# Performance work log

Measured on AMD Instinct MI355X. Metric: run time of the kernel, lower is better.

Reference implementation:

```python
import jax, jax.numpy as jnp
import numpy as np

C = 4096      # channels_in == channels_out == Cn (deg rows)
K = 3         # dynamic kernel size
RED = 8       # CA reduction
CH, CW = 64, 64  # reshape_codebooks(4096) -> (sqrt(4096), sqrt(4096)); must equal feature H, W


def leaky(x):
    return jnp.where(x >= 0, x, 0.1 * x)  # LeakyReLU(0.1)


def setup_inputs() -> dict:
    key = jax.random.key(0)
    ks = jax.random.split(key, 8)
    s = 0.02
    return {
        "c": jax.random.normal(ks[0], (1, C, CH, CW), jnp.float32),      # feature map B,C,H,W (B=1 required)
        "deg": jax.random.normal(ks[1], (C, C), jnp.float32),            # degradation reps Cn x C
        "W1": jax.random.normal(ks[2], (C, C), jnp.float32) * s,         # kernel MLP: Linear(C,C,bias=False) weight (out,in)
        "W2": jax.random.normal(ks[3], (K * K, C), jnp.float32) * s,     # kernel MLP: Linear(C,K*K,bias=False)
        "Wc": jax.random.normal(ks[4], (C, C), jnp.float32) * s,         # 1x1 conv weight (out,in)
        "bc": jnp.zeros((C,), jnp.float32),                              # 1x1 conv bias
        "Wd1": jax.random.normal(ks[5], (C // RED, C), jnp.float32) * s, # CA conv1 1x1 (out,in)
        "Wd2": jax.random.normal(ks[6], (C, C // RED), jnp.float32) * s, # CA conv2 1x1 (out,in)
    }


def reference(c, deg, W1, W2, Wc, bc, Wd1, Wd2):
    b, cc, h, w = c.shape
    # --- dynamic per-channel kernel generation: Linear -> LeakyReLU -> Linear ---
    kern = leaky(deg @ W1.T) @ W2.T                      # (b*c, K*K)
    kern = kern.reshape(b * cc, 1, K, K)                 # depthwise weights (O, 1, K, K)
    # --- depthwise grouped conv with groups = b*c ---
    pad = (K - 1) // 2
    x = c.reshape(1, b * cc, h, w)
    out = jax.lax.conv_general_dilated(
        x, kern, window_strides=(1, 1), padding=((pad, pad), (pad, pad)),
        feature_group_count=b * cc, dimension_numbers=('NCHW', 'OIHW', 'NCHW'))
    out = leaky(out).reshape(b, cc, h, w)
    # --- 1x1 conv (channels_in -> channels_out) ---
    out = jnp.einsum('oc,bchw->bohw', Wc, out) + bc[None, :, None, None]
    # --- channel attention branch on deg ---
    d = deg.reshape(1, C, CH, CW)
    hid = leaky(jnp.einsum('oc,bchw->bohw', Wd1, d))     # (1, C//RED, CH, CW)
    att = jax.nn.sigmoid(jnp.einsum('oc,bchw->bohw', Wd2, hid))  # (1, C, CH, CW)
    return out + d * att
```

## Files before the change

kernel.cpp:

```cpp
#include <hip/hip_runtime.h>
#include <stdint.h>

typedef unsigned short u16;
typedef __attribute__((ext_vector_type(8))) short bf16x8;
typedef __attribute__((ext_vector_type(4))) float f32x4;

static __device__ __forceinline__ u16 f2bf(float f) {
  uint32_t u = __float_as_uint(f);
  return (u16)((u + 0x7fffu + ((u >> 16) & 1u)) >> 16);
}
static __device__ __forceinline__ float bf2f(u16 h) {
  return __uint_as_float(((uint32_t)h) << 16);
}

static __device__ __forceinline__ void gload_lds16(const void* g, void* l) {
  __builtin_amdgcn_global_load_lds((const __attribute__((address_space(1))) void*)g,
                                   (__attribute__((address_space(3))) void*)l, 16, 0, 0);
}

__global__ __launch_bounds__(256) void cast_bf16_kernel(const float* __restrict__ in,
                                                        u16* __restrict__ out, int n4) {
  int idx = blockIdx.x * 256 + threadIdx.x;
  if (idx >= n4) return;
  float4 v = ((const float4*)in)[idx];
  u16 o0 = f2bf(v.x), o1 = f2bf(v.y), o2 = f2bf(v.z), o3 = f2bf(v.w);
  uint2 packed;
  packed.x = (uint32_t)o0 | ((uint32_t)o1 << 16);
  packed.y = (uint32_t)o2 | ((uint32_t)o3 << 16);
  ((uint2*)out)[idx] = packed;
}

__global__ __launch_bounds__(256) void deg_prep_kernel(const float* __restrict__ in,
                                                       u16* __restrict__ degb,
                                                       u16* __restrict__ degt) {
  __shared__ float t[64][72];
  const int r0 = blockIdx.y * 64, c0 = blockIdx.x * 64;
  const int tid = threadIdx.x;
  const int rr = tid >> 4;
  const int c4 = (tid & 15) * 4;
#pragma unroll
  for (int s = 0; s < 4; ++s) {
    const int row = r0 + rr + s * 16;
    float4 v = *(const float4*)&in[(size_t)row * 4096 + c0 + c4];
    *(float4*)&t[rr + s * 16][c4] = v;
    uint2 p;
    p.x = (uint32_t)f2bf(v.x) | ((uint32_t)f2bf(v.y) << 16);
    p.y = (uint32_t)f2bf(v.z) | ((uint32_t)f2bf(v.w) << 16);
    *(uint2*)&degb[(size_t)row * 4096 + c0 + c4] = p;
  }
  __syncthreads();
  const int oc = tid >> 2;
  const int or16 = (tid & 3) * 16;
  bf16x8 o0, o1;
#pragma unroll
  for (int u = 0; u < 8; ++u) o0[u] = (short)f2bf(t[or16 + u][oc]);
#pragma unroll
  for (int u = 0; u < 8; ++u) o1[u] = (short)f2bf(t[or16 + 8 + u][oc]);
  *(bf16x8*)&degt[(size_t)(c0 + oc) * 4096 + r0 + or16] = o0;
  *(bf16x8*)&degt[(size_t)(c0 + oc) * 4096 + r0 + or16 + 8] = o1;
}

__global__ __launch_bounds__(256) void transpose_bf16_kernel(const u16* __restrict__ in,
                                                             u16* __restrict__ out) {
  __shared__ u16 t[64][72];
  const int r0 = blockIdx.y * 64, c0 = blockIdx.x * 64;
  const int tid = threadIdx.x;
  const int rr = tid >> 3;
  const int c8 = (tid & 7) * 8;
#pragma unroll
  for (int s = 0; s < 2; ++s) {
    bf16x8 v = *(const bf16x8*)&in[(size_t)(r0 + rr + s * 32) * 4096 + c0 + c8];
    *(bf16x8*)&t[rr + s * 32][c8] = v;
  }
  __syncthreads();
  const int oc = tid >> 2;
  const int or16 = (tid & 3) * 16;
  bf16x8 o0, o1;
#pragma unroll
  for (int u = 0; u < 8; ++u) o0[u] = (short)t[or16 + u][oc];
#pragma unroll
  for (int u = 0; u < 8; ++u) o1[u] = (short)t[or16 + 8 + u][oc];
  *(bf16x8*)&out[(size_t)(c0 + oc) * 4096 + r0 + or16] = o0;
  *(bf16x8*)&out[(size_t)(c0 + oc) * 4096 + r0 + or16 + 8] = o1;
}

__global__ __launch_bounds__(256) void combine_leaky_kernel(const float* __restrict__ P,
                                                            u16* __restrict__ out, int n4) {
  int idx = blockIdx.x * 256 + threadIdx.x;
  if (idx >= n4) return;
  float4 a = ((const float4*)P)[idx];
  float4 b = ((const float4*)(P + (size_t)4096 * 512))[idx];
  float s0 = a.x + b.x, s1 = a.y + b.y, s2 = a.z + b.z, s3 = a.w + b.w;
  s0 = s0 >= 0.f ? s0 : 0.1f * s0;
  s1 = s1 >= 0.f ? s1 : 0.1f * s1;
  s2 = s2 >= 0.f ? s2 : 0.1f * s2;
  s3 = s3 >= 0.f ? s3 : 0.1f * s3;
  uint2 p;
  p.x = (uint32_t)f2bf(s0) | ((uint32_t)f2bf(s1) << 16);
  p.y = (uint32_t)f2bf(s2) | ((uint32_t)f2bf(s3) << 16);
  ((uint2*)out)[idx] = p;
}

__global__ __launch_bounds__(256) void kern_reduce_kernel(const u16* __restrict__ H,
                                                          const float* __restrict__ W2,
                                                          float* __restrict__ kern) {
  const int i = blockIdx.x;
  const int tid = threadIdx.x;
  float acc[9];
#pragma unroll
  for (int t = 0; t < 9; ++t) acc[t] = 0.f;
#pragma unroll
  for (int it = 0; it < 2; ++it) {
    const int j = (it * 256 + tid) * 8;
    bf16x8 hv = *(const bf16x8*)&H[(size_t)i * 4096 + j];
    float hf[8];
#pragma unroll
    for (int u = 0; u < 8; ++u) hf[u] = bf2f((u16)hv[u]);
#pragma unroll
    for (int t = 0; t < 9; ++t) {
      float s = 0.f;
#pragma unroll
      for (int u = 0; u < 8; ++u) s += hf[u] * W2[t * 4096 + j + u];
      acc[t] += s;
    }
  }
  __shared__ float red[4 * 9];
  const int lane = tid & 63, wid = tid >> 6;
#pragma unroll
  for (int t = 0; t < 9; ++t) {
    float v = acc[t];
#pragma unroll
    for (int off = 32; off > 0; off >>= 1) v += __shfl_down(v, off);
    if (lane == 0) red[wid * 9 + t] = v;
  }
  __syncthreads();
  if (tid < 9) kern[(size_t)i * 9 + tid] = red[tid] + red[9 + tid] + red[18 + tid] + red[27 + tid];
}

__global__ __launch_bounds__(256) void dwconv_kernel(const float* __restrict__ x,
                                                     const float* __restrict__ kern,
                                                     u16* __restrict__ V) {
  const int ch = blockIdx.x;
  __shared__ float img[4096];
  const float* src = x + (size_t)ch * 4096;
#pragma unroll
  for (int s = 0; s < 4; ++s)
    ((float4*)img)[s * 256 + threadIdx.x] = ((const float4*)src)[s * 256 + threadIdx.x];
  float kv[9];
#pragma unroll
  for (int t = 0; t < 9; ++t) kv[t] = kern[(size_t)ch * 9 + t];
  __syncthreads();
#pragma unroll
  for (int s = 0; s < 16; ++s) {
    const int p = s * 256 + threadIdx.x;
    const int h = p >> 6, w = p & 63;
    float sum = 0.f;
#pragma unroll
    for (int dh = -1; dh <= 1; ++dh) {
      const int hh = h + dh;
      if ((unsigned)hh < 64u) {
#pragma unroll
        for (int dw = -1; dw <= 1; ++dw) {
          const int wwi = w + dw;
          if ((unsigned)wwi < 64u) sum += img[hh * 64 + wwi] * kv[(dh + 1) * 3 + (dw + 1)];
        }
      }
    }
    sum = sum >= 0.f ? sum : 0.1f * sum;
    V[(size_t)ch * 4096 + p] = f2bf(sum);
  }
}

template <int EPI>
__global__ __launch_bounds__(256, 4) void gemm_nt(const u16* __restrict__ A,
                                                  const u16* __restrict__ B,
                                                  void* __restrict__ Cout,
                                                  int M, int N, int K,
                                                  const float* __restrict__ bias,
                                                  const float* __restrict__ degf,
                                                  const u16* __restrict__ att) {
  __shared__ u16 Asm[128 * 64];
  __shared__ u16 Bsm[128 * 64];
  const int tid = threadIdx.x;
  const int lane = tid & 63;
  const int wid = tid >> 6;
  const int wr = wid >> 1, wc = wid & 1;
  const int nwg = gridDim.x * gridDim.y;
  int lin = blockIdx.y * gridDim.x + blockIdx.x;
  lin = (lin & 7) * (nwg >> 3) + (lin >> 3);
  const int bn = (lin % gridDim.x) * 128;
  const int bm = (lin / gridDim.x) * 128;
  const int kper = K / gridDim.z;
  const int k0 = blockIdx.z * kper, k1 = k0 + kper;

  const int srow = tid >> 3;
  const int sseg = tid & 7;
  const int ssw  = (sseg ^ (srow & 7)) * 8;
  const int l15 = lane & 15;
  const int seg0 = lane >> 4;
  const int lx7 = l15 & 7;

  f32x4 acc[4][4];
#pragma unroll
  for (int m = 0; m < 4; ++m)
#pragma unroll
    for (int n = 0; n < 4; ++n) acc[m][n] = (f32x4){0.f, 0.f, 0.f, 0.f};

  const size_t aBase = (size_t)bm * K;
  const size_t bBase = (size_t)bn * K;

  for (int kt = k0; kt < k1; kt += 64) {
    __syncthreads();
#pragma unroll
    for (int bi = 0; bi < 4; ++bi) {
      const u16* ga = A + aBase + (size_t)(bi * 32 + srow) * K + kt + ssw;
      gload_lds16(ga, &Asm[(bi * 32 + srow) * 64 + sseg * 8]);
      const u16* gb = B + bBase + (size_t)(bi * 32 + srow) * K + kt + ssw;
      gload_lds16(gb, &Bsm[(bi * 32 + srow) * 64 + sseg * 8]);
    }
    __syncthreads();
#pragma unroll
    for (int ks = 0; ks < 2; ++ks) {
      bf16x8 av[4], bv[4];
#pragma unroll
      for (int m = 0; m < 4; ++m)
        av[m] = *(const bf16x8*)&Asm[(wr * 64 + m * 16 + l15) * 64 +
                                     (((ks * 4 + seg0) ^ lx7) * 8)];
#pragma unroll
      for (int n = 0; n < 4; ++n)
        bv[n] = *(const bf16x8*)&Bsm[(wc * 64 + n * 16 + l15) * 64 +
                                     (((ks * 4 + seg0) ^ lx7) * 8)];
#pragma unroll
      for (int m = 0; m < 4; ++m)
#pragma unroll
        for (int n = 0; n < 4; ++n)
          acc[m][n] = __builtin_amdgcn_mfma_f32_16x16x32_bf16(av[m], bv[n], acc[m][n], 0, 0, 0);
    }
  }

#pragma unroll
  for (int m = 0; m < 4; ++m) {
    const int row0 = bm + wr * 64 + m * 16 + (lane >> 4) * 4;
#pragma unroll
    for (int n = 0; n < 4; ++n) {
      const int col = bn + wc * 64 + n * 16 + l15;
#pragma unroll
      for (int j = 0; j < 4; ++j) {
        const int row = row0 + j;
        float v = acc[m][n][j];
        const size_t idx = (size_t)row * N + col;
        if (EPI == 0) {
          v = v >= 0.f ? v : 0.1f * v;
          ((u16*)Cout)[idx] = f2bf(v);
        } else if (EPI == 1) {
          v = 1.f / (1.f + __expf(-v));
          ((u16*)Cout)[idx] = f2bf(v);
        } else if (EPI == 2) {
          v += bias[row] + degf[idx] * bf2f(att[idx]);
          ((float*)Cout)[idx] = v;
        } else {
          ((float*)Cout)[(size_t)blockIdx.z * ((size_t)M * N) + idx] = v;
        }
      }
    }
  }
}

extern "C" void kernel_launch(void* const* d_in, const int* in_sizes, int n_in,
                              void* d_out, int out_size, void* d_ws, size_t ws_size,
                              hipStream_t stream) {
  const float* xc  = (const float*)d_in[0];
  const float* deg = (const float*)d_in[1];
  const float* W1  = (const float*)d_in[2];
  const float* W2  = (const float*)d_in[3];
  const float* Wc  = (const float*)d_in[4];
  const float* bc  = (const float*)d_in[5];
  const float* Wd1 = (const float*)d_in[6];
  const float* Wd2 = (const float*)d_in[7];
  float* out = (float*)d_out;

  char* ws = (char*)d_ws;
  const size_t MB = 1ull << 20;
  u16* RA    = (u16*)(ws + 0 * MB);
  u16* RB    = (u16*)(ws + 32 * MB);
  u16* RC    = (u16*)(ws + 64 * MB);
  u16* ATT   = (u16*)(ws + 96 * MB);
  u16* WD1B  = (u16*)(ws + 128 * MB);
  u16* WD2B  = (u16*)(ws + 132 * MB);
  u16* HIDT  = (u16*)(ws + 136 * MB);
  float* KERN = (float*)(ws + 140 * MB);

  cast_bf16_kernel<<<2048, 256, 0, stream>>>(Wd1, WD1B, 512 * 4096 / 4);
  cast_bf16_kernel<<<2048, 256, 0, stream>>>(Wd2, WD2B, 4096 * 512 / 4);
  deg_prep_kernel<<<dim3(64, 64), 256, 0, stream>>>(deg, RB, RA);
  gemm_nt<3><<<dim3(4, 32, 2), 256, 0, stream>>>(RA, WD1B, (float*)RC, 4096, 512, 4096,
                                                 nullptr, nullptr, nullptr);
  combine_leaky_kernel<<<2048, 256, 0, stream>>>((const float*)RC, HIDT, 4096 * 512 / 4);
  gemm_nt<1><<<dim3(32, 32), 256, 0, stream>>>(WD2B, HIDT, ATT, 4096, 4096, 512,
                                               nullptr, nullptr, nullptr);

  cast_bf16_kernel<<<16384, 256, 0, stream>>>(W1, RA, 4096 * 4096 / 4);
  gemm_nt<0><<<dim3(32, 32), 256, 0, stream>>>(RB, RA, RC, 4096, 4096, 4096,
                                               nullptr, nullptr, nullptr);
  kern_reduce_kernel<<<4096, 256, 0, stream>>>(RC, W2, KERN);

  dwconv_kernel<<<4096, 256, 0, stream>>>(xc, KERN, RA);
  transpose_bf16_kernel<<<dim3(64, 64), 256, 0, stream>>>(RA, RB);

  cast_bf16_kernel<<<16384, 256, 0, stream>>>(Wc, RC, 4096 * 4096 / 4);
  gemm_nt<2><<<dim3(32, 32), 256, 0, stream>>>(RC, RB, out, 4096, 4096, 4096,
                                               bc, deg, ATT);
}
```

Baseline: 492.7 us.

## Fuse W2 kernel reduction into GEMM epilogue and read deg as bf16

The W1 GEMM epilogue now applies LeakyReLU and immediately contracts each row tile with W2. It writes 9-wide partial sums per column slice, and a small kernel sums the 64 slices. This replaces the full 4096x4096 bf16 hidden matrix write, its re-read and the old per-row reduction kernel. The final GEMM epilogue reads the bf16 copy of deg instead of the fp32 input, halving that traffic at some precision cost. The Wd1 GEMM also goes to 4-way split-K with a 4-slice combine. The fused epilogue adds per-element FMAs against W2 loads from global memory, plus cross-lane shuffles.

```diff
diff --git a/kernel.cpp b/kernel.cpp
--- a/kernel.cpp
+++ b/kernel.cpp
@@ -88,9 +88,15 @@
                                                             u16* __restrict__ out, int n4) {
   int idx = blockIdx.x * 256 + threadIdx.x;
   if (idx >= n4) return;
+  const size_t SL = (size_t)4096 * 512;
   float4 a = ((const float4*)P)[idx];
-  float4 b = ((const float4*)(P + (size_t)4096 * 512))[idx];
-  float s0 = a.x + b.x, s1 = a.y + b.y, s2 = a.z + b.z, s3 = a.w + b.w;
+  float4 b = ((const float4*)(P + SL))[idx];
+  float4 c = ((const float4*)(P + 2 * SL))[idx];
+  float4 d = ((const float4*)(P + 3 * SL))[idx];
+  float s0 = (a.x + b.x) + (c.x + d.x);
+  float s1 = (a.y + b.y) + (c.y + d.y);
+  float s2 = (a.z + b.z) + (c.z + d.z);
+  float s3 = (a.w + b.w) + (c.w + d.w);
   s0 = s0 >= 0.f ? s0 : 0.1f * s0;
   s1 = s1 >= 0.f ? s1 : 0.1f * s1;
   s2 = s2 >= 0.f ? s2 : 0.1f * s2;
@@ -101,40 +107,14 @@
   ((uint2*)out)[idx] = p;
 }
 
-__global__ __launch_bounds__(256) void kern_reduce_kernel(const u16* __restrict__ H,
-                                                          const float* __restrict__ W2,
-                                                          float* __restrict__ kern) {
-  const int i = blockIdx.x;
-  const int tid = threadIdx.x;
-  float acc[9];
-#pragma unroll
-  for (int t = 0; t < 9; ++t) acc[t] = 0.f;
-#pragma unroll
-  for (int it = 0; it < 2; ++it) {
-    const int j = (it * 256 + tid) * 8;
-    bf16x8 hv = *(const bf16x8*)&H[(size_t)i * 4096 + j];
-    float hf[8];
-#pragma unroll
-    for (int u = 0; u < 8; ++u) hf[u] = bf2f((u16)hv[u]);
-#pragma unroll
-    for (int t = 0; t < 9; ++t) {
-      float s = 0.f;
-#pragma unroll
-      for (int u = 0; u < 8; ++u) s += hf[u] * W2[t * 4096 + j + u];
-      acc[t] += s;
-    }
-  }
-  __shared__ float red[4 * 9];
-  const int lane = tid & 63, wid = tid >> 6;
-#pragma unroll
-  for (int t = 0; t < 9; ++t) {
-    float v = acc[t];
-#pragma unroll
-    for (int off = 32; off > 0; off >>= 1) v += __shfl_down(v, off);
-    if (lane == 0) red[wid * 9 + t] = v;
-  }
-  __syncthreads();
-  if (tid < 9) kern[(size_t)i * 9 + tid] = red[tid] + red[9 + tid] + red[18 + tid] + red[27 + tid];
+__global__ __launch_bounds__(256) void kpart_reduce_kernel(const float* __restrict__ kp,
+                                                           float* __restrict__ kern) {
+  int idx = blockIdx.x * 256 + threadIdx.x;
+  if (idx >= 4096 * 9) return;
+  float s = 0.f;
+#pragma unroll
+  for (int sl = 0; sl < 64; ++sl) s += kp[(size_t)sl * 36864 + idx];
+  kern[idx] = s;
 }
 
 __global__ __launch_bounds__(256) void dwconv_kernel(const float* __restrict__ x,
@@ -177,8 +157,8 @@
                                                   void* __restrict__ Cout,
                                                   int M, int N, int K,
                                                   const float* __restrict__ bias,
-                                                  const float* __restrict__ degf,
-                                                  const u16* __restrict__ att) {
+                                                  const u16* __restrict__ att,
+                                                  const u16* __restrict__ degb) {
   __shared__ u16 Asm[128 * 64];
   __shared__ u16 Bsm[128 * 64];
   const int tid = threadIdx.x;
@@ -238,28 +218,57 @@
     }
   }
 
-#pragma unroll
-  for (int m = 0; m < 4; ++m) {
-    const int row0 = bm + wr * 64 + m * 16 + (lane >> 4) * 4;
-#pragma unroll
-    for (int n = 0; n < 4; ++n) {
-      const int col = bn + wc * 64 + n * 16 + l15;
-#pragma unroll
-      for (int j = 0; j < 4; ++j) {
-        const int row = row0 + j;
-        float v = acc[m][n][j];
-        const size_t idx = (size_t)row * N + col;
-        if (EPI == 0) {
+  if (EPI == 4) {
+    const int g = lane >> 4;
+    float* kp = (float*)Cout + (size_t)((bn >> 7) * 2 + wc) * 36864;
+#pragma unroll
+    for (int m = 0; m < 4; ++m) {
+#pragma unroll
+      for (int jr = 0; jr < 4; ++jr) {
+        const int i = bm + wr * 64 + m * 16 + g * 4 + jr;
+        float s[9];
+#pragma unroll
+        for (int t = 0; t < 9; ++t) s[t] = 0.f;
+#pragma unroll
+        for (int n = 0; n < 4; ++n) {
+          float v = acc[m][n][jr];
           v = v >= 0.f ? v : 0.1f * v;
-          ((u16*)Cout)[idx] = f2bf(v);
-        } else if (EPI == 1) {
-          v = 1.f / (1.f + __expf(-v));
-          ((u16*)Cout)[idx] = f2bf(v);
-        } else if (EPI == 2) {
-          v += bias[row] + degf[idx] * bf2f(att[idx]);
-          ((float*)Cout)[idx] = v;
-        } else {
-          ((float*)Cout)[(size_t)blockIdx.z * ((size_t)M * N) + idx] = v;
+          const int col = bn + wc * 64 + n * 16 + l15;
+#pragma unroll
+          for (int t = 0; t < 9; ++t) s[t] += v * bias[t * 4096 + col];
+        }
+#pragma unroll
+        for (int off = 1; off < 16; off <<= 1) {
+#pragma unroll
+          for (int t = 0; t < 9; ++t) s[t] += __shfl_xor(s[t], off);
+        }
+        if (l15 == 0) {
+#pragma unroll
+          for (int t = 0; t < 9; ++t) kp[(size_t)i * 9 + t] = s[t];
+        }
+      }
+    }
+  } else {
+#pragma unroll
+    for (int m = 0; m < 4; ++m) {
+      const int row0 = bm + wr * 64 + m * 16 + (lane >> 4) * 4;
+#pragma unroll
+      for (int n = 0; n < 4; ++n) {
+        const int col = bn + wc * 64 + n * 16 + l15;
+#pragma unroll
+        for (int j = 0; j < 4; ++j) {
+          const int row = row0 + j;
+          float v = acc[m][n][j];
+          const size_t idx = (size_t)row * N + col;
+          if (EPI == 1) {
+            v = 1.f / (1.f + __expf(-v));
+            ((u16*)Cout)[idx] = f2bf(v);
+          } else if (EPI == 3) {
+            ((float*)Cout)[(size_t)blockIdx.z * ((size_t)M * N) + idx] = v;
+          } else {
+            v += bias[row] + bf2f(degb[idx]) * bf2f(att[idx]);
+            ((float*)Cout)[idx] = v;
+          }
         }
       }
     }
@@ -284,7 +293,7 @@
   u16* RA    = (u16*)(ws + 0 * MB);
   u16* RB    = (u16*)(ws + 32 * MB);
   u16* RC    = (u16*)(ws + 64 * MB);
-  u16* ATT   = (u16*)(ws + 96 * MB);
+  u16* RATT  = (u16*)(ws + 96 * MB);
   u16* WD1B  = (u16*)(ws + 128 * MB);
   u16* WD2B  = (u16*)(ws + 132 * MB);
   u16* HIDT  = (u16*)(ws + 136 * MB);
@@ -293,21 +302,21 @@
   cast_bf16_kernel<<<2048, 256, 0, stream>>>(Wd1, WD1B, 512 * 4096 / 4);
   cast_bf16_kernel<<<2048, 256, 0, stream>>>(Wd2, WD2B, 4096 * 512 / 4);
   deg_prep_kernel<<<dim3(64, 64), 256, 0, stream>>>(deg, RB, RA);
-  gemm_nt<3><<<dim3(4, 32, 2), 256, 0, stream>>>(RA, WD1B, (float*)RC, 4096, 512, 4096,
+  gemm_nt<3><<<dim3(4, 32, 4), 256, 0, stream>>>(RA, WD1B, (float*)RC, 4096, 512, 4096,
                                                  nullptr, nullptr, nullptr);
   combine_leaky_kernel<<<2048, 256, 0, stream>>>((const float*)RC, HIDT, 4096 * 512 / 4);
-  gemm_nt<1><<<dim3(32, 32), 256, 0, stream>>>(WD2B, HIDT, ATT, 4096, 4096, 512,
+  gemm_nt<1><<<dim3(32, 32), 256, 0, stream>>>(WD2B, HIDT, RATT, 4096, 4096, 512,
                                                nullptr, nullptr, nullptr);
 
   cast_bf16_kernel<<<16384, 256, 0, stream>>>(W1, RA, 4096 * 4096 / 4);
-  gemm_nt<0><<<dim3(32, 32), 256, 0, stream>>>(RB, RA, RC, 4096, 4096, 4096,
-                                               nullptr, nullptr, nullptr);
-  kern_reduce_kernel<<<4096, 256, 0, stream>>>(RC, W2, KERN);
+  gemm_nt<4><<<dim3(32, 32), 256, 0, stream>>>(RB, RA, (float*)RC, 4096, 4096, 4096,
+                                               W2, nullptr, nullptr);
+  kpart_reduce_kernel<<<144, 256, 0, stream>>>((const float*)RC, KERN);
 
   dwconv_kernel<<<4096, 256, 0, stream>>>(xc, KERN, RA);
-  transpose_bf16_kernel<<<dim3(64, 64), 256, 0, stream>>>(RA, RB);
-
-  cast_bf16_kernel<<<16384, 256, 0, stream>>>(Wc, RC, 4096 * 4096 / 4);
-  gemm_nt<2><<<dim3(32, 32), 256, 0, stream>>>(RC, RB, out, 4096, 4096, 4096,
-                                               bc, deg, ATT);
-}
+  transpose_bf16_kernel<<<dim3(64, 64), 256, 0, stream>>>(RA, RC);
+
+  cast_bf16_kernel<<<16384, 256, 0, stream>>>(Wc, RA, 4096 * 4096 / 4);
+  gemm_nt<5><<<dim3(32, 32), 256, 0, stream>>>(RA, RC, out, 4096, 4096, 4096,
+                                               bc, RATT, RB);
+}
```

Result: slower. 523.0 us (+6.2%).

## Add 256x256 eight-wave pipelined GEMM for deg@W1 and raise split-K for CA

Applied to the files above, without the earlier changes.

Replaces the generic gemm_nt<0> for the 4096^3 deg@W1 product with a new 256x256-tile, 512-thread kernel. It uses direct global-to-LDS loads with XOR-swizzled rows, double-buffered 128KB LDS, explicit waitcnt and barrier phasing, setprio around MFMA bursts, and a fused LeakyReLU bf16 epilogue. It also raises the split-K of the Wd1 GEMM from 2 to 4, with the combine kernel now summing four partials, and vectorises kern_reduce loads. The aim is better MFMA utilisation and latency hiding on the largest GEMM. The cost is one workgroup per CU and hand-tuned sync that depends on exact sizes.

```diff
diff --git a/kernel.cpp b/kernel.cpp
--- a/kernel.cpp
+++ b/kernel.cpp
@@ -16,6 +16,12 @@
 static __device__ __forceinline__ void gload_lds16(const void* g, void* l) {
   __builtin_amdgcn_global_load_lds((const __attribute__((address_space(1))) void*)g,
                                    (__attribute__((address_space(3))) void*)l, 16, 0, 0);
+}
+
+static __device__ __forceinline__ bf16x8 dsr128(uint32_t byteaddr) {
+  bf16x8 r;
+  asm volatile("ds_read_b128 %0, %1" : "=v"(r) : "v"(byteaddr));
+  return r;
 }
 
 __global__ __launch_bounds__(256) void cast_bf16_kernel(const float* __restrict__ in,
@@ -88,9 +94,15 @@
                                                             u16* __restrict__ out, int n4) {
   int idx = blockIdx.x * 256 + threadIdx.x;
   if (idx >= n4) return;
+  const size_t SL = (size_t)4096 * 512;
   float4 a = ((const float4*)P)[idx];
-  float4 b = ((const float4*)(P + (size_t)4096 * 512))[idx];
-  float s0 = a.x + b.x, s1 = a.y + b.y, s2 = a.z + b.z, s3 = a.w + b.w;
+  float4 b = ((const float4*)(P + SL))[idx];
+  float4 c = ((const float4*)(P + 2 * SL))[idx];
+  float4 d = ((const float4*)(P + 3 * SL))[idx];
+  float s0 = (a.x + b.x) + (c.x + d.x);
+  float s1 = (a.y + b.y) + (c.y + d.y);
+  float s2 = (a.z + b.z) + (c.z + d.z);
+  float s3 = (a.w + b.w) + (c.w + d.w);
   s0 = s0 >= 0.f ? s0 : 0.1f * s0;
   s1 = s1 >= 0.f ? s1 : 0.1f * s1;
   s2 = s2 >= 0.f ? s2 : 0.1f * s2;
@@ -110,18 +122,15 @@
 #pragma unroll
   for (int t = 0; t < 9; ++t) acc[t] = 0.f;
 #pragma unroll
-  for (int it = 0; it < 2; ++it) {
-    const int j = (it * 256 + tid) * 8;
-    bf16x8 hv = *(const bf16x8*)&H[(size_t)i * 4096 + j];
-    float hf[8];
-#pragma unroll
-    for (int u = 0; u < 8; ++u) hf[u] = bf2f((u16)hv[u]);
+  for (int it = 0; it < 4; ++it) {
+    const int j = it * 1024 + tid * 4;
+    uint2 hv = *(const uint2*)&H[(size_t)i * 4096 + j];
+    float h0 = bf2f((u16)(hv.x & 0xffff)), h1 = bf2f((u16)(hv.x >> 16));
+    float h2 = bf2f((u16)(hv.y & 0xffff)), h3 = bf2f((u16)(hv.y >> 16));
 #pragma unroll
     for (int t = 0; t < 9; ++t) {
-      float s = 0.f;
-#pragma unroll
-      for (int u = 0; u < 8; ++u) s += hf[u] * W2[t * 4096 + j + u];
-      acc[t] += s;
+      float4 w = *(const float4*)&W2[t * 4096 + j];
+      acc[t] += h0 * w.x + h1 * w.y + h2 * w.z + h3 * w.w;
     }
   }
   __shared__ float red[4 * 9];
@@ -266,6 +275,124 @@
   }
 }
 
+template __global__ void gemm_nt<0>(const u16*, const u16*, void*, int, int, int,
+                                    const float*, const float*, const u16*);
+
+#define PH4(P, BUFB, READB, S1, S2, TAILV)                                         \
+  {                                                                                \
+    bf16x8 af[4][2];                                                               \
+    _Pragma("unroll") for (int f = 0; f < 4; ++f) {                                \
+      af[f][0] = dsr128((BUFB) + arow + (uint32_t)(((P) * 4 + f) * 2048) + sg0);   \
+      af[f][1] = dsr128((BUFB) + arow + (uint32_t)(((P) * 4 + f) * 2048) + sg1);   \
+    }                                                                              \
+    if (READB) {                                                                   \
+      _Pragma("unroll") for (int nf = 0; nf < 4; ++nf) {                           \
+        bfr[nf][0] = dsr128((BUFB) + brow + (uint32_t)(nf * 2048) + sg0);          \
+        bfr[nf][1] = dsr128((BUFB) + brow + (uint32_t)(nf * 2048) + sg1);          \
+      }                                                                            \
+    }                                                                              \
+    S1; S2;                                                                        \
+    __builtin_amdgcn_s_barrier();                                                  \
+    asm volatile("s_waitcnt lgkmcnt(0)" ::: "memory");                             \
+    __builtin_amdgcn_sched_barrier(0);                                             \
+    __builtin_amdgcn_s_setprio(1);                                                 \
+    _Pragma("unroll") for (int f = 0; f < 4; ++f)                                  \
+      _Pragma("unroll") for (int nf = 0; nf < 4; ++nf)                             \
+        _Pragma("unroll") for (int ks = 0; ks < 2; ++ks)                           \
+          acc[(P) * 4 + f][nf] = __builtin_amdgcn_mfma_f32_16x16x32_bf16(          \
+              af[f][ks], bfr[nf][ks], acc[(P) * 4 + f][nf], 0, 0, 0);              \
+    __builtin_amdgcn_s_setprio(0);                                                 \
+    __builtin_amdgcn_sched_barrier(0);                                             \
+    TAILV;                                                                         \
+    __builtin_amdgcn_s_barrier();                                                  \
+  }
+#define VM4 asm volatile("s_waitcnt vmcnt(4)" ::: "memory")
+#define VM0 asm volatile("s_waitcnt vmcnt(0)" ::: "memory")
+
+__global__ __launch_bounds__(512, 1) void gemm8p4(const u16* __restrict__ A,
+                                                  const u16* __restrict__ B,
+                                                  u16* __restrict__ Cout,
+                                                  int N, int K, int gx) {
+  extern __shared__ u16 lds[];
+  const int tid = threadIdx.x;
+  const int lane = tid & 63;
+  const int w = tid >> 6;
+  const int wr = w >> 2, wcn = w & 3;
+
+  const int nwg = gridDim.x;
+  const int cpx = nwg >> 3;
+  const int swz = (blockIdx.x & 7) * cpx + (blockIdx.x >> 3);
+  const int bn = (swz % gx) * 256;
+  const int bm = (swz / gx) * 256;
+
+  const int srow = tid >> 3;
+  const int sseg = tid & 7;
+  const int ssrc = (sseg ^ (srow & 7)) * 8;
+
+  const int l15 = lane & 15, g = lane >> 4;
+  const uint32_t sg0 = (uint32_t)(((0 + g) ^ (l15 & 7)) * 16);
+  const uint32_t sg1 = (uint32_t)(((4 + g) ^ (l15 & 7)) * 16);
+  const uint32_t arow = (uint32_t)((wr * 128 + l15) * 128);
+  const uint32_t brow = (uint32_t)((wcn * 64 + l15) * 128) + 32768u;
+
+  const u16* Ab = A + (size_t)(bm + srow) * K + ssrc;
+  const u16* Bb = B + (size_t)(bn + srow) * K + ssrc;
+
+  auto stage = [&](const u16* Mb, uint32_t bufbyte, int t, int half) {
+#pragma unroll
+    for (int r = 0; r < 2; ++r) {
+      const int rowl = half * 128 + r * 64 + srow;
+      gload_lds16(Mb + (size_t)(half * 128 + r * 64) * K + (size_t)t * 64,
+                  (char*)lds + bufbyte + (uint32_t)(rowl * 128 + sseg * 16));
+    }
+  };
+
+  f32x4 acc[8][4];
+#pragma unroll
+  for (int m = 0; m < 8; ++m)
+#pragma unroll
+    for (int n = 0; n < 4; ++n) acc[m][n] = (f32x4){0.f, 0.f, 0.f, 0.f};
+  bf16x8 bfr[4][2];
+
+  const int NIT = K >> 7;
+
+  stage(Bb, 32768u, 0, 0); stage(Bb, 32768u, 0, 1);
+  stage(Ab, 0u, 0, 0);     stage(Ab, 0u, 0, 1);
+  stage(Bb, 98304u, 1, 0); stage(Bb, 98304u, 1, 1);
+  VM4;
+  __builtin_amdgcn_s_barrier();
+
+  for (int i = 0; i < NIT - 1; ++i) {
+    const int to = 2 * i + 1, te = 2 * i + 2, tn = 2 * i + 3;
+    PH4(0, 0u, 1, stage(Ab, 65536u, to, 0), stage(Ab, 65536u, to, 1), );
+    PH4(1, 0u, 0, stage(Bb, 32768u, te, 0), stage(Bb, 32768u, te, 1), VM4);
+    PH4(0, 65536u, 1, stage(Ab, 0u, te, 0), stage(Ab, 0u, te, 1), );
+    PH4(1, 65536u, 0, stage(Bb, 98304u, tn, 0), stage(Bb, 98304u, tn, 1), VM4);
+  }
+  {
+    const int to = 2 * (NIT - 1) + 1;
+    PH4(0, 0u, 1, stage(Ab, 65536u, to, 0), stage(Ab, 65536u, to, 1), );
+    PH4(1, 0u, 0, , , VM0);
+    PH4(0, 65536u, 1, , , );
+    PH4(1, 65536u, 0, , , );
+  }
+
+#pragma unroll
+  for (int mf = 0; mf < 8; ++mf) {
+    const int row0 = bm + wr * 128 + mf * 16 + (lane >> 4) * 4;
+#pragma unroll
+    for (int nf = 0; nf < 4; ++nf) {
+      const int col = bn + wcn * 64 + nf * 16 + l15;
+#pragma unroll
+      for (int j = 0; j < 4; ++j) {
+        float v = acc[mf][nf][j];
+        v = v >= 0.f ? v : 0.1f * v;
+        Cout[(size_t)(row0 + j) * N + col] = f2bf(v);
+      }
+    }
+  }
+}
+
 extern "C" void kernel_launch(void* const* d_in, const int* in_sizes, int n_in,
                               void* d_out, int out_size, void* d_ws, size_t ws_size,
                               hipStream_t stream) {
@@ -284,24 +411,25 @@
   u16* RA    = (u16*)(ws + 0 * MB);
   u16* RB    = (u16*)(ws + 32 * MB);
   u16* RC    = (u16*)(ws + 64 * MB);
-  u16* ATT   = (u16*)(ws + 96 * MB);
+  u16* RATT  = (u16*)(ws + 96 * MB);
   u16* WD1B  = (u16*)(ws + 128 * MB);
   u16* WD2B  = (u16*)(ws + 132 * MB);
   u16* HIDT  = (u16*)(ws + 136 * MB);
   float* KERN = (float*)(ws + 140 * MB);
 
+  hipFuncSetAttribute((const void*)gemm8p4, hipFuncAttributeMaxDynamicSharedMemorySize, 131072);
+
   cast_bf16_kernel<<<2048, 256, 0, stream>>>(Wd1, WD1B, 512 * 4096 / 4);
   cast_bf16_kernel<<<2048, 256, 0, stream>>>(Wd2, WD2B, 4096 * 512 / 4);
   deg_prep_kernel<<<dim3(64, 64), 256, 0, stream>>>(deg, RB, RA);
-  gemm_nt<3><<<dim3(4, 32, 2), 256, 0, stream>>>(RA, WD1B, (float*)RC, 4096, 512, 4096,
+  gemm_nt<3><<<dim3(4, 32, 4), 256, 0, stream>>>(RA, WD1B, (float*)RC, 4096, 512, 4096,
                                                  nullptr, nullptr, nullptr);
   combine_leaky_kernel<<<2048, 256, 0, stream>>>((const float*)RC, HIDT, 4096 * 512 / 4);
-  gemm_nt<1><<<dim3(32, 32), 256, 0, stream>>>(WD2B, HIDT, ATT, 4096, 4096, 512,
+  gemm_nt<1><<<dim3(32, 32), 256, 0, stream>>>(WD2B, HIDT, RATT, 4096, 4096, 512,
                                                nullptr, nullptr, nullptr);
 
   cast_bf16_kernel<<<16384, 256, 0, stream>>>(W1, RA, 4096 * 4096 / 4);
-  gemm_nt<0><<<dim3(32, 32), 256, 0, stream>>>(RB, RA, RC, 4096, 4096, 4096,
-                                               nullptr, nullptr, nullptr);
+  gemm8p4<<<256, 512, 131072, stream>>>(RB, RA, RC, 4096, 4096, 16);
   kern_reduce_kernel<<<4096, 256, 0, stream>>>(RC, W2, KERN);
 
   dwconv_kernel<<<4096, 256, 0, stream>>>(xc, KERN, RA);
@@ -309,5 +437,5 @@
 
   cast_bf16_kernel<<<16384, 256, 0, stream>>>(Wc, RC, 4096 * 4096 / 4);
   gemm_nt<2><<<dim3(32, 32), 256, 0, stream>>>(RC, RB, out, 4096, 4096, 4096,
-                                               bc, deg, ATT);
-}
+                                               bc, deg, RATT);
+}
```

After: 615.1 us. +24.8%, slower.
